# Kernel tuning notes

Hardware: AMD Instinct MI355X
Metric: run time of the kernel (lower is better)

Reference implementation:

```python
import jax, jax.numpy as jnp
import numpy as np

N, E, G = 20000, 640000, 64
D_IN, H, C, D_OUT = 256, 4, 64, 32
HC = H * C


def gat_layer(x, W, a_src, a_dst, b, src, dst, n_nodes, heads, ch):
    # x: [N, F_in], W: [F_in, H*C]
    h = (x @ W).reshape(n_nodes, heads, ch)          # [N,H,C]
    es = jnp.einsum('nhc,hc->nh', h, a_src)          # [N,H]
    ed = jnp.einsum('nhc,hc->nh', h, a_dst)
    e = jax.nn.leaky_relu(es[src] + ed[dst], 0.2)    # [Etot,H]
    m = jax.ops.segment_max(e, dst, num_segments=n_nodes)
    m = jnp.where(jnp.isfinite(m), m, 0.0)
    ex = jnp.exp(e - m[dst])
    denom = jax.ops.segment_sum(ex, dst, num_segments=n_nodes)
    alpha = ex / jnp.maximum(denom[dst], 1e-16)      # softmax over in-edges per dst
    out = jax.ops.segment_sum(alpha[:, :, None] * h[src], dst, num_segments=n_nodes)
    return out.reshape(n_nodes, heads * ch) + b


def setup_inputs() -> dict:
    key = jax.random.key(0)
    ks = jax.random.split(key, 14)
    g1 = 1.0 / np.sqrt(D_IN)
    g2 = 1.0 / np.sqrt(HC)
    inp = {
        'x': jax.random.normal(ks[0], (N, D_IN), jnp.float32),
        'edge_index': jax.random.randint(ks[1], (2, E), 0, N, jnp.int64 if jax.config.jax_enable_x64 else jnp.int32),
        'batch': jnp.sort(jax.random.randint(ks[2], (N,), 0, G)),
        'W1': jax.random.normal(ks[3], (D_IN, HC), jnp.float32) * g1,
        'a_src1': jax.random.normal(ks[4], (H, C), jnp.float32) * g2,
        'a_dst1': jax.random.normal(ks[5], (H, C), jnp.float32) * g2,
        'b1': jnp.zeros((HC,), jnp.float32),
        'W2': jax.random.normal(ks[6], (HC, HC), jnp.float32) * g2,
        'a_src2': jax.random.normal(ks[7], (H, C), jnp.float32) * g2,
        'a_dst2': jax.random.normal(ks[8], (H, C), jnp.float32) * g2,
        'b2': jnp.zeros((HC,), jnp.float32),
        'Wp': jax.random.normal(ks[9], (HC, D_OUT), jnp.float32) * g2,
        'bp': jnp.zeros((D_OUT,), jnp.float32),
    }
    return inp


def reference(x, edge_index, batch, W1, a_src1, a_dst1, b1, W2, a_src2, a_dst2, b2, Wp, bp):
    # add self-loops (PyG GATConv default)
    loop = jnp.arange(N, dtype=edge_index.dtype)
    src = jnp.concatenate([edge_index[0], loop])
    dst = jnp.concatenate([edge_index[1], loop])
    x1 = jax.nn.relu(gat_layer(x, W1, a_src1, a_dst1, b1, src, dst, N, H, C))
    # dropout p=0.6 is identity in eval mode
    x2 = jax.nn.relu(gat_layer(x1, W2, a_src2, a_dst2, b2, src, dst, N, H, C))
    node_scores = x2 @ Wp + bp                        # [N, D_OUT]
    sums = jax.ops.segment_sum(node_scores, batch, num_segments=G)
    counts = jax.ops.segment_sum(jnp.ones((N,), node_scores.dtype), batch, num_segments=G)
    return sums / jnp.maximum(counts, 1.0)[:, None]   # [G, D_OUT]
```

## Files before the change

### kernel.cpp

```cpp
#include <hip/hip_runtime.h>
#include <hip/hip_bf16.h>
#include <cstdint>

#define NNODES 20000
#define NEDGES 640000
#define ETOT   (NEDGES + NNODES)
#define NGROUP 64
#define HC     256
#define DOUT   32

typedef short bf16x8 __attribute__((ext_vector_type(8)));
typedef short s16x4  __attribute__((ext_vector_type(4)));
typedef float f32x4  __attribute__((ext_vector_type(4)));

__device__ __forceinline__ float b2f(__hip_bfloat16 v) { return __bfloat162float(v); }
__device__ __forceinline__ float bs2f(short v) {
    union { unsigned int u; float f; } c; c.u = ((unsigned int)(unsigned short)v) << 16; return c.f;
}
__device__ __forceinline__ short f2bs(float v) {
    __hip_bfloat16 b = __float2bfloat16(v);
    union { __hip_bfloat16 b; short s; } u; u.b = b; return u.s;
}
__device__ __forceinline__ float ldf(const void* __restrict__ p, size_t i, int bf) {
    return bf ? __bfloat162float(((const __hip_bfloat16*)p)[i]) : ((const float*)p)[i];
}
__device__ __forceinline__ int ld_idx(const int* __restrict__ p, size_t i, int f64) {
    return f64 ? p[2 * i] : p[i];
}

__global__ void k_probe(const unsigned int* __restrict__ xw, const int* __restrict__ ei,
                        int* __restrict__ flag, int* __restrict__ deg) {
    int t = blockIdx.x * 256 + threadIdx.x;
    for (int i = t; i < NNODES; i += 256 * 32) deg[i] = 0;
    if (blockIdx.x == 0 && threadIdx.x < 64) {
        int l = threadIdx.x;
        int ones = 0, zeros = 0;
#pragma unroll
        for (int r = 0; r < 4; r++) {
            unsigned long long b1 = __ballot((xw[r * 64 + l] >> 14) & 1);
            unsigned long long b2 = __ballot(ei[2 * (r * 64 + l) + 1] == 0);
            ones  += __popcll(b1);
            zeros += __popcll(b2);
        }
        if (l == 0) { flag[1] = (ones < 64) ? 1 : 0; flag[0] = (zeros > 200) ? 1 : 0; }
    }
}

__global__ void k_hist(const int* __restrict__ ei, int* __restrict__ deg,
                       const int* __restrict__ flag) {
    int i = blockIdx.x * blockDim.x + threadIdx.x;
    if (i >= ETOT) return;
    int f = flag[0];
    int d = (i < NEDGES) ? ld_idx(ei, (size_t)NEDGES + i, f) : (i - NEDGES);
    atomicAdd(&deg[d], 1);
}

__global__ void k_scan(const int* __restrict__ deg, int* __restrict__ off, int* __restrict__ cur,
                       float* __restrict__ sx, int* __restrict__ cnt) {
    __shared__ int wsum[8];
    int t = threadIdx.x, lane = t & 63, wv = t >> 6;
    for (int i = t; i < NGROUP * HC; i += 512) sx[i] = 0.f;
    if (t < NGROUP) cnt[t] = 0;
    const int CH = ((NNODES + 511) / 512) * 64;
    int base = wv * CH;
    int s = 0;
    for (int i0 = 0; i0 < CH; i0 += 64) {
        int i = base + i0 + lane;
        s += (i < NNODES) ? deg[i] : 0;
    }
#pragma unroll
    for (int o = 1; o < 64; o <<= 1) s += __shfl_xor(s, o);
    if (lane == 0) wsum[wv] = s;
    __syncthreads();
    int run = 0;
    for (int i = 0; i < wv; i++) run += wsum[i];
    for (int i0 = 0; i0 < CH; i0 += 64) {
        int i = base + i0 + lane;
        int v = (i < NNODES) ? deg[i] : 0;
        int sc = v;
#pragma unroll
        for (int o = 1; o < 64; o <<= 1) {
            int u = __shfl_up(sc, o);
            if (lane >= o) sc += u;
        }
        if (i < NNODES) { int ex = run + sc - v; off[i] = ex; cur[i] = ex; }
        run += __shfl(sc, 63);
    }
    if (t == 0) off[NNODES] = ETOT;
}

__global__ void k_scatter(const int* __restrict__ ei, int* __restrict__ cur,
                          int* __restrict__ csr, const int* __restrict__ flag) {
    int i = blockIdx.x * blockDim.x + threadIdx.x;
    if (i >= ETOT) return;
    int f = flag[0];
    int s, d;
    if (i < NEDGES) { s = ld_idx(ei, i, f); d = ld_idx(ei, (size_t)NEDGES + i, f); }
    else            { s = d = i - NEDGES; }
    int pos = atomicAdd(&cur[d], 1);
    csr[pos] = s;
}

__global__ void k_wt(const void* __restrict__ W1, const void* __restrict__ W2,
                     __hip_bfloat16* __restrict__ Wt1, __hip_bfloat16* __restrict__ Wt2,
                     const int* __restrict__ flag) {
    int i = blockIdx.x * 256 + threadIdx.x;
    int which = i >> 16;
    int j = i & 65535;
    int k = j >> 8, n = j & 255;
    const void* W = which ? W2 : W1;
    __hip_bfloat16* Wt = which ? Wt2 : Wt1;
    Wt[(size_t)n * 256 + k] = __float2bfloat16(ldf(W, (size_t)k * 256 + n, flag[1]));
}

__global__ __launch_bounds__(256) void k_gemm(const void* __restrict__ A,
                                              const __hip_bfloat16* __restrict__ Bt,
                                              __hip_bfloat16* __restrict__ Hout,
                                              const void* __restrict__ a_src,
                                              const void* __restrict__ a_dst,
                                              float* __restrict__ es4, float* __restrict__ ed4,
                                              const int* __restrict__ flag, int force_bf) {
    int bf   = flag[1];
    int abf  = force_bf | bf;
    int w    = threadIdx.x >> 6;
    int lane = threadIdx.x & 63;
    int mr   = lane & 15;
    int quad = lane >> 4;
    int r0   = blockIdx.x * 16;
    if (r0 >= NNODES) return;
    f32x4 acc[4];
#pragma unroll
    for (int j = 0; j < 4; j++) acc[j] = (f32x4){0.f, 0.f, 0.f, 0.f};
    size_t rowoff = (size_t)(r0 + mr) * HC;
    const __hip_bfloat16* Btw = Bt + (size_t)w * 64 * HC;
    for (int kk = 0; kk < HC; kk += 32) {
        bf16x8 a;
        if (abf) {
            a = *reinterpret_cast<const bf16x8*>((const __hip_bfloat16*)A + rowoff + kk + quad * 8);
        } else {
            const float* af = (const float*)A + rowoff + kk + quad * 8;
            f32x4 lo = *reinterpret_cast<const f32x4*>(af);
            f32x4 hi = *reinterpret_cast<const f32x4*>(af + 4);
#pragma unroll
            for (int ii = 0; ii < 4; ii++) { a[ii] = f2bs(lo[ii]); a[ii + 4] = f2bs(hi[ii]); }
        }
#pragma unroll
        for (int j = 0; j < 4; j++) {
            bf16x8 b = *reinterpret_cast<const bf16x8*>(Btw + (size_t)(j * 16 + mr) * HC + kk + quad * 8);
            acc[j] = __builtin_amdgcn_mfma_f32_16x16x32_bf16(a, b, acc[j], 0, 0, 0);
        }
    }
#pragma unroll
    for (int j = 0; j < 4; j++)
#pragma unroll
        for (int r = 0; r < 4; r++)
            Hout[(size_t)(r0 + quad * 4 + r) * HC + w * 64 + j * 16 + mr] = __float2bfloat16(acc[j][r]);
    float ps[4] = {0.f, 0.f, 0.f, 0.f}, pd[4] = {0.f, 0.f, 0.f, 0.f};
#pragma unroll
    for (int j = 0; j < 4; j++) {
        float asv = ldf(a_src, (size_t)(w * 64 + j * 16 + mr), bf);
        float adv = ldf(a_dst, (size_t)(w * 64 + j * 16 + mr), bf);
#pragma unroll
        for (int r = 0; r < 4; r++) {
            ps[r] = fmaf(acc[j][r], asv, ps[r]);
            pd[r] = fmaf(acc[j][r], adv, pd[r]);
        }
    }
#pragma unroll
    for (int o = 1; o < 16; o <<= 1)
#pragma unroll
        for (int r = 0; r < 4; r++) {
            ps[r] += __shfl_xor(ps[r], o);
            pd[r] += __shfl_xor(pd[r], o);
        }
    if (mr == 0)
#pragma unroll
        for (int r = 0; r < 4; r++) {
            int row = r0 + quad * 4 + r;
            es4[(size_t)row * 4 + w] = ps[r];
            ed4[(size_t)row * 4 + w] = pd[r];
        }
}

__global__ __launch_bounds__(256) void k_agg(const __hip_bfloat16* __restrict__ Hb,
                                             const float* __restrict__ es4, const float* __restrict__ ed4,
                                             const void* __restrict__ bias,
                                             const int* __restrict__ off, const int* __restrict__ csr,
                                             const int* __restrict__ flag,
                                             __hip_bfloat16* __restrict__ out) {
    __shared__ float p_lds[4][256];
    __shared__ int   s_lds[4][64];
    int wv = threadIdx.x >> 6;
    int l  = threadIdx.x & 63;
    int n  = blockIdx.x * 4 + wv;
    int hd = l >> 4;
    int base = off[n], deg = off[n + 1] - base;
    f32x4 edv = *reinterpret_cast<const f32x4*>(ed4 + (size_t)n * 4);
    f32x4 m    = (f32x4){-INFINITY, -INFINITY, -INFINITY, -INFINITY};
    f32x4 dsum = (f32x4){0.f, 0.f, 0.f, 0.f};
    f32x4 acc  = (f32x4){0.f, 0.f, 0.f, 0.f};
    for (int c0 = 0; c0 < deg; c0 += 64) {
        int cn = min(deg - c0, 64);
        f32x4 ev;
        if (l < cn) {
            int s = csr[base + c0 + l];
            s_lds[wv][l] = s;
            f32x4 e = *reinterpret_cast<const f32x4*>(es4 + (size_t)s * 4);
#pragma unroll
            for (int h = 0; h < 4; h++) {
                float t = e[h] + edv[h];
                ev[h] = (t > 0.f) ? t : 0.2f * t;
            }
        } else {
#pragma unroll
            for (int h = 0; h < 4; h++) ev[h] = -INFINITY;
        }
        f32x4 mc = ev;
#pragma unroll
        for (int o = 32; o; o >>= 1)
#pragma unroll
            for (int h = 0; h < 4; h++) mc[h] = fmaxf(mc[h], __shfl_xor(mc[h], o));
        f32x4 al, pv;
#pragma unroll
        for (int h = 0; h < 4; h++) {
            float nm = fmaxf(m[h], mc[h]);
            al[h] = __expf(m[h] - nm);
            m[h]  = nm;
        }
#pragma unroll
        for (int h = 0; h < 4; h++) pv[h] = (l < cn) ? __expf(ev[h] - m[h]) : 0.f;
        f32x4 sc = pv;
#pragma unroll
        for (int o = 32; o; o >>= 1)
#pragma unroll
            for (int h = 0; h < 4; h++) sc[h] += __shfl_xor(sc[h], o);
#pragma unroll
        for (int h = 0; h < 4; h++) dsum[h] = dsum[h] * al[h] + sc[h];
        acc *= al[hd];
        *reinterpret_cast<f32x4*>(&p_lds[wv][l * 4]) = pv;
        int jm = cn & ~7;
        for (int j = 0; j < jm; j += 8) {
            s16x4 hv[8];
            float pj[8];
#pragma unroll
            for (int i = 0; i < 8; i++) {
                int sj = s_lds[wv][j + i];
                hv[i] = *reinterpret_cast<const s16x4*>(Hb + (size_t)sj * HC + l * 4);
                pj[i] = p_lds[wv][(j + i) * 4 + hd];
            }
#pragma unroll
            for (int i = 0; i < 8; i++)
#pragma unroll
                for (int k = 0; k < 4; k++) acc[k] = fmaf(pj[i], bs2f(hv[i][k]), acc[k]);
        }
        for (int j = jm; j < cn; j++) {
            int sj  = s_lds[wv][j];
            float p = p_lds[wv][j * 4 + hd];
            s16x4 hv = *reinterpret_cast<const s16x4*>(Hb + (size_t)sj * HC + l * 4);
#pragma unroll
            for (int k = 0; k < 4; k++) acc[k] = fmaf(p, bs2f(hv[k]), acc[k]);
        }
    }
    float dd = fmaxf(dsum[hd], 1e-16f);
    int bf = flag[1];
    s16x4 ov;
#pragma unroll
    for (int k = 0; k < 4; k++) {
        float v = acc[k] / dd + ldf(bias, (size_t)l * 4 + k, bf);
        ov[k] = f2bs(fmaxf(v, 0.f));
    }
    *reinterpret_cast<s16x4*>(out + (size_t)n * HC + l * 4) = ov;
}

__global__ __launch_bounds__(256) void k_groupsum(const __hip_bfloat16* __restrict__ X2,
                                                  const int* __restrict__ batch,
                                                  float* __restrict__ sx, int* __restrict__ cnt,
                                                  const int* __restrict__ flag) {
    const int RPB = NNODES / 250;
    int b = blockIdx.x, f = flag[0];
    int sub = threadIdx.x >> 6, l = threadIdx.x & 63;
    int r = b * RPB + sub;
    f32x4 acc = (f32x4){0.f, 0.f, 0.f, 0.f};
    int curg = ld_idx(batch, r, f);
    int cacc = 0;
    for (int k = 0; k < RPB / 4; k++, r += 4) {
        int g = ld_idx(batch, r, f);
        if (g != curg) {
#pragma unroll
            for (int c = 0; c < 4; c++) atomicAdd(&sx[(size_t)curg * HC + l * 4 + c], acc[c]);
            if (l == 0) atomicAdd(&cnt[curg], cacc);
            acc = (f32x4){0.f, 0.f, 0.f, 0.f}; cacc = 0; curg = g;
        }
        s16x4 hv = *reinterpret_cast<const s16x4*>(X2 + (size_t)r * HC + l * 4);
#pragma unroll
        for (int c = 0; c < 4; c++) acc[c] += bs2f(hv[c]);
        cacc++;
    }
#pragma unroll
    for (int c = 0; c < 4; c++) atomicAdd(&sx[(size_t)curg * HC + l * 4 + c], acc[c]);
    if (l == 0) atomicAdd(&cnt[curg], cacc);
}

__global__ __launch_bounds__(256) void k_final(const float* __restrict__ sx,
                                               const void* __restrict__ Wp,
                                               const void* __restrict__ bp,
                                               const int* __restrict__ cnt,
                                               const int* __restrict__ flag,
                                               void* __restrict__ out) {
    __shared__ float red[8][32];
    int g = blockIdx.x, t = threadIdx.x;
    int c = t & 31, seg = t >> 5;
    int bf = flag[1];
    const float* sxg = sx + (size_t)g * HC;
    float a = 0.f;
#pragma unroll
    for (int k = 0; k < 32; k++) {
        int kk = seg * 32 + k;
        a = fmaf(sxg[kk], ldf(Wp, (size_t)kk * DOUT + c, bf), a);
    }
    red[seg][c] = a;
    __syncthreads();
    if (t < 32) {
        float s = 0.f;
#pragma unroll
        for (int i = 0; i < 8; i++) s += red[i][t];
        int ct = cnt[g];
        float v = (ct > 0) ? (s / ct + ldf(bp, (size_t)t, bf)) : 0.f;
        if (bf) ((__hip_bfloat16*)out)[g * DOUT + t] = __float2bfloat16(v);
        else    ((float*)out)[g * DOUT + t]          = v;
    }
}

extern "C" void kernel_launch(void* const* d_in, const int* in_sizes, int n_in,
                              void* d_out, int out_size, void* d_ws, size_t ws_size,
                              hipStream_t stream) {
    (void)in_sizes; (void)n_in; (void)out_size; (void)ws_size;
    const void* x   = d_in[0];
    const int*  ei  = (const int*)d_in[1];
    const int*  bat = (const int*)d_in[2];
    const void* W1  = d_in[3];
    const void* as1 = d_in[4];
    const void* ad1 = d_in[5];
    const void* b1  = d_in[6];
    const void* W2  = d_in[7];
    const void* as2 = d_in[8];
    const void* ad2 = d_in[9];
    const void* b2  = d_in[10];
    const void* Wp  = d_in[11];
    const void* bp  = d_in[12];

    char* ws = (char*)d_ws;
    size_t o = 0;
    auto alloc = [&](size_t bytes) -> char* {
        char* p = ws + o;
        o += (bytes + 255) & ~(size_t)255;
        return p;
    };
    __hip_bfloat16* hb  = (__hip_bfloat16*)alloc((size_t)NNODES * HC * 2);
    __hip_bfloat16* xb  = (__hip_bfloat16*)alloc((size_t)NNODES * HC * 2);
    __hip_bfloat16* xb2 = (__hip_bfloat16*)alloc((size_t)NNODES * HC * 2);
    __hip_bfloat16* Wt1 = (__hip_bfloat16*)alloc((size_t)HC * HC * 2);
    __hip_bfloat16* Wt2 = (__hip_bfloat16*)alloc((size_t)HC * HC * 2);
    float* es = (float*)alloc((size_t)NNODES * 4 * 4);
    float* ed = (float*)alloc((size_t)NNODES * 4 * 4);
    int* deg  = (int*)alloc((size_t)NNODES * 4);
    int* cur  = (int*)alloc((size_t)NNODES * 4);
    int* off  = (int*)alloc((size_t)(NNODES + 1) * 4);
    int* csr  = (int*)alloc((size_t)ETOT * 4);
    float* sx = (float*)alloc((size_t)NGROUP * HC * 4);
    int* cnt  = (int*)alloc(256);
    int* flag = (int*)alloc(256);

    k_probe<<<32, 256, 0, stream>>>((const unsigned int*)x, ei, flag, deg);
    k_hist<<<(ETOT + 255) / 256, 256, 0, stream>>>(ei, deg, flag);
    k_scan<<<1, 512, 0, stream>>>(deg, off, cur, sx, cnt);
    k_scatter<<<(ETOT + 255) / 256, 256, 0, stream>>>(ei, cur, csr, flag);
    k_wt<<<512, 256, 0, stream>>>(W1, W2, Wt1, Wt2, flag);

    k_gemm<<<NNODES / 16, 256, 0, stream>>>(x, Wt1, hb, as1, ad1, es, ed, flag, 0);
    k_agg<<<NNODES / 4, 256, 0, stream>>>(hb, es, ed, b1, off, csr, flag, xb);

    k_gemm<<<NNODES / 16, 256, 0, stream>>>(xb, Wt2, hb, as2, ad2, es, ed, flag, 1);
    k_agg<<<NNODES / 4, 256, 0, stream>>>(hb, es, ed, b2, off, csr, flag, xb2);

    k_groupsum<<<250, 256, 0, stream>>>(xb2, bat, sx, cnt, flag);
    k_final<<<NGROUP, 256, 0, stream>>>(sx, Wp, bp, cnt, flag, d_out);
}
```

Measured before the change: 349.3 us.

## Split wave into two half-waves gathering 16-byte rows for alternating edges

The aggregation kernel now has each half-wave (32 lanes) load a full 256-channel bf16 row with 16-byte vector loads, and the two halves handle even and odd edges. Their partial accumulators are combined with a cross-half shuffle at the end. This widens the per-lane gather loads and doubles the number of edges in flight per iteration, aiming to raise memory-level parallelism in the neighbour gather. The tail loop is removed by padding chunks to 16 edges. Padded slots read node 0 with zero weight, and the per-lane accumulator registers double from 4 to 8.

```diff
diff --git a/kernel.cpp b/kernel.cpp
--- a/kernel.cpp
+++ b/kernel.cpp
@@ -193,18 +193,22 @@
     int wv = threadIdx.x >> 6;
     int l  = threadIdx.x & 63;
     int n  = blockIdx.x * 4 + wv;
-    int hd = l >> 4;
+    int half = l >> 5;
+    int hl   = l & 31;
+    int hd8  = hl >> 3;
     int base = off[n], deg = off[n + 1] - base;
     f32x4 edv = *reinterpret_cast<const f32x4*>(ed4 + (size_t)n * 4);
     f32x4 m    = (f32x4){-INFINITY, -INFINITY, -INFINITY, -INFINITY};
     f32x4 dsum = (f32x4){0.f, 0.f, 0.f, 0.f};
-    f32x4 acc  = (f32x4){0.f, 0.f, 0.f, 0.f};
+    float acc[8];
+#pragma unroll
+    for (int k = 0; k < 8; k++) acc[k] = 0.f;
     for (int c0 = 0; c0 < deg; c0 += 64) {
         int cn = min(deg - c0, 64);
+        int s = (l < cn) ? csr[base + c0 + l] : 0;
+        s_lds[wv][l] = s;
         f32x4 ev;
         if (l < cn) {
-            int s = csr[base + c0 + l];
-            s_lds[wv][l] = s;
             f32x4 e = *reinterpret_cast<const f32x4*>(es4 + (size_t)s * 4);
 #pragma unroll
             for (int h = 0; h < 4; h++) {
@@ -236,40 +240,41 @@
             for (int h = 0; h < 4; h++) sc[h] += __shfl_xor(sc[h], o);
 #pragma unroll
         for (int h = 0; h < 4; h++) dsum[h] = dsum[h] * al[h] + sc[h];
-        acc *= al[hd];
+        float a8 = al[hd8];
+#pragma unroll
+        for (int k = 0; k < 8; k++) acc[k] *= a8;
         *reinterpret_cast<f32x4*>(&p_lds[wv][l * 4]) = pv;
-        int jm = cn & ~7;
-        for (int j = 0; j < jm; j += 8) {
-            s16x4 hv[8];
+        int jn = (cn + 15) & ~15;
+        for (int j = 0; j < jn; j += 16) {
+            bf16x8 hv[8];
             float pj[8];
 #pragma unroll
             for (int i = 0; i < 8; i++) {
-                int sj = s_lds[wv][j + i];
-                hv[i] = *reinterpret_cast<const s16x4*>(Hb + (size_t)sj * HC + l * 4);
-                pj[i] = p_lds[wv][(j + i) * 4 + hd];
+                int e  = j + 2 * i + half;
+                int sj = s_lds[wv][e];
+                hv[i] = *reinterpret_cast<const bf16x8*>(Hb + (size_t)sj * HC + hl * 8);
+                pj[i] = p_lds[wv][e * 4 + hd8];
             }
 #pragma unroll
             for (int i = 0; i < 8; i++)
 #pragma unroll
-                for (int k = 0; k < 4; k++) acc[k] = fmaf(pj[i], bs2f(hv[i][k]), acc[k]);
-        }
-        for (int j = jm; j < cn; j++) {
-            int sj  = s_lds[wv][j];
-            float p = p_lds[wv][j * 4 + hd];
-            s16x4 hv = *reinterpret_cast<const s16x4*>(Hb + (size_t)sj * HC + l * 4);
-#pragma unroll
-            for (int k = 0; k < 4; k++) acc[k] = fmaf(p, bs2f(hv[k]), acc[k]);
-        }
-    }
-    float dd = fmaxf(dsum[hd], 1e-16f);
+                for (int k = 0; k < 8; k++) acc[k] = fmaf(pj[i], bs2f(hv[i][k]), acc[k]);
+        }
+    }
+#pragma unroll
+    for (int k = 0; k < 8; k++) acc[k] += __shfl_xor(acc[k], 32);
+    float dd = fmaxf(dsum[hd8], 1e-16f);
+    float rin = 1.0f / dd;
     int bf = flag[1];
-    s16x4 ov;
-#pragma unroll
-    for (int k = 0; k < 4; k++) {
-        float v = acc[k] / dd + ldf(bias, (size_t)l * 4 + k, bf);
-        ov[k] = f2bs(fmaxf(v, 0.f));
-    }
-    *reinterpret_cast<s16x4*>(out + (size_t)n * HC + l * 4) = ov;
+    if (half == 0) {
+        bf16x8 ov;
+#pragma unroll
+        for (int k = 0; k < 8; k++) {
+            float v = acc[k] * rin + ldf(bias, (size_t)hl * 8 + k, bf);
+            ov[k] = f2bs(fmaxf(v, 0.f));
+        }
+        *reinterpret_cast<bf16x8*>(out + (size_t)n * HC + hl * 8) = ov;
+    }
 }
 
 __global__ __launch_bounds__(256) void k_groupsum(const __hip_bfloat16* __restrict__ X2,
```

After: 351.1 us. No clear change (+0.5%).
